# Optimization experiments

Measured on AMD Instinct MI355X. Metric: run time of the kernel, lower is better.

## Reference

```python
import jax, jax.numpy as jnp
import numpy as np

N_BLADES = 8  # Cl(3,0): 1, e1, e2, e3 and their products (bitmask blade indexing)


def _blade_sign(a: int, b: int) -> int:
    # Sign from reordering basis vectors when multiplying blades a*b (Euclidean metric).
    a >>= 1
    s = 0
    while a:
        s += bin(a & b).count('1')
        a >>= 1
    return -1 if (s & 1) else 1


def make_cayley() -> np.ndarray:
    C = np.zeros((N_BLADES, N_BLADES, N_BLADES), dtype=np.float32)
    for a in range(N_BLADES):
        for b in range(N_BLADES):
            C[a, b, a ^ b] = float(_blade_sign(a, b))
    return C


def setup_inputs() -> dict:
    key = jax.random.key(0)
    k1, k2 = jax.random.split(key)
    B, Cin, Cout = 8192, 256, 256
    scale = 1.0 / np.sqrt(Cin * N_BLADES)
    x = jax.random.normal(k1, (B, Cin, N_BLADES), dtype=jnp.float32)
    weight = jax.random.normal(k2, (Cout, Cin, N_BLADES), dtype=jnp.float32) * scale
    bias = jnp.zeros((Cout, N_BLADES), dtype=jnp.float32)
    cayley = jnp.asarray(make_cayley())
    return {"x": x, "weight": weight, "bias": bias, "cayley": cayley}


def reference(x, weight, bias, cayley):
    # A[b,o,j,k] = sum_i W[o,i,j] * X[b,i,k]  (weight blade j times input blade k)
    A = jnp.einsum('oij,bik->bojk', weight, x)
    # Contract blade pair (j,k) into output blade l via sparse Cayley table.
    out = jnp.einsum('jkl,bojk->bol', cayley, A)
    return out + bias[None, :, :]
```

## Files before the change

kernel.cpp:

```cpp
#include <hip/hip_runtime.h>
#include <stdint.h>
#include <stddef.h>


typedef __bf16 bf16x8  __attribute__((ext_vector_type(8)));
typedef float  f32x4   __attribute__((ext_vector_type(4)));

#define BM 256
#define BN 256
#define KSLICE 32
#define NSLICES 64
#define SLOT_ELEMS (256 * 32)

__device__ __forceinline__ void async_copy16(void* lds_dst, const void* g_src) {
    __builtin_amdgcn_global_load_lds(
        (__attribute__((address_space(1))) void*)g_src,
        (__attribute__((address_space(3))) void*)lds_dst,
        16, 0, 0);
}

__global__ __launch_bounds__(256) void prep_kernel(
    const float* __restrict__ x, __bf16* __restrict__ Xb, long nx,
    const float* __restrict__ W, const float* __restrict__ cayley,
    __bf16* __restrict__ Wt, int Cin, int Cout, int castBlocks)
{
    __shared__ float Cay[512];
    if ((int)blockIdx.x < castBlocks) {
        long i = ((long)blockIdx.x * 256 + threadIdx.x) * 8;
        if (i + 8 <= nx) {
            const f32x4* p = (const f32x4*)(x + i);
            f32x4 v0 = p[0];
            f32x4 v1 = p[1];
            bf16x8 o;
            o[0] = (__bf16)v0[0]; o[1] = (__bf16)v0[1];
            o[2] = (__bf16)v0[2]; o[3] = (__bf16)v0[3];
            o[4] = (__bf16)v1[0]; o[5] = (__bf16)v1[1];
            o[6] = (__bf16)v1[2]; o[7] = (__bf16)v1[3];
            *(bf16x8*)(Xb + i) = o;
        }
        return;
    }
    for (int t = threadIdx.x; t < 512; t += 256) Cay[t] = cayley[t];
    __syncthreads();

    int flat = (blockIdx.x - castBlocks) * 256 + threadIdx.x;
    int total = Cout * 8 * Cin;
    if (flat >= total) return;
    int i = flat % Cin;
    int n = flat / Cin;
    int o = n >> 3, l = n & 7;

    const float* wrow = W + ((size_t)o * Cin + i) * 8;
    float w8[8];
    #pragma unroll
    for (int j = 0; j < 8; ++j) w8[j] = wrow[j];

    bf16x8 outv;
    #pragma unroll
    for (int k = 0; k < 8; ++k) {
        float s = 0.f;
        #pragma unroll
        for (int j = 0; j < 8; ++j) s += Cay[j * 64 + k * 8 + l] * w8[j];
        outv[k] = (__bf16)s;
    }
    *(bf16x8*)(Wt + (size_t)n * (Cin * 8) + i * 8) = outv;
}

__global__ __launch_bounds__(512, 2) void gemm_bt_kernel(
    const __bf16* __restrict__ A,
    const __bf16* __restrict__ Bt,
    const float*  __restrict__ bias,
    float* __restrict__ C,
    int M, int N, int K)
{
    __shared__ __align__(16) __bf16 As[4][SLOT_ELEMS];
    __shared__ __align__(16) __bf16 Bs[4][SLOT_ELEMS];

    const int tid  = threadIdx.x;
    const int wave = tid >> 6;
    const int lane = tid & 63;
    const int quad = lane >> 4;
    const int l16  = lane & 15;

    const int bid = blockIdx.x;
    const int xcd = bid & 7;
    const int idx = bid >> 3;
    const int mBase = (xcd * 4 + (idx & 3)) * BM;
    const int nBase = (idx >> 2) * BN;

    const int srow = lane >> 2;
    const int sgrp = (lane & 3) ^ ((lane >> 3) & 3);
    const __bf16* gA0 = A  + (size_t)(mBase + wave * 32 +  0 + srow) * K + sgrp * 8;
    const __bf16* gA1 = A  + (size_t)(mBase + wave * 32 + 16 + srow) * K + sgrp * 8;
    const __bf16* gB0 = Bt + (size_t)(nBase + wave * 32 +  0 + srow) * K + sgrp * 8;
    const __bf16* gB1 = Bt + (size_t)(nBase + wave * 32 + 16 + srow) * K + sgrp * 8;
    const int stOff = wave * 1024;

#define STAGE_A(slot, q) do {                                             \
        async_copy16(&As[slot][stOff      ], gA0 + (size_t)(q) * KSLICE); \
        async_copy16(&As[slot][stOff + 512], gA1 + (size_t)(q) * KSLICE); \
    } while (0)
#define STAGE_B(slot, q) do {                                             \
        async_copy16(&Bs[slot][stOff      ], gB0 + (size_t)(q) * KSLICE); \
        async_copy16(&Bs[slot][stOff + 512], gB1 + (size_t)(q) * KSLICE); \
    } while (0)

    const int wm = wave >> 2;
    const int wn = wave & 3;
    const int offq = (quad ^ ((l16 >> 1) & 3)) * 8;
    const __bf16* paBase = &As[0][(wm * 128 + l16) * KSLICE + offq];
    const __bf16* pbBase = &Bs[0][(wn * 64  + l16) * KSLICE + offq];

    f32x4 acc[8][4] = {};
    bf16x8 af0A[4], bfA[4], af0B[4], bfB[4], af1[4];

    STAGE_A(0, 0); STAGE_B(0, 0);
    STAGE_A(1, 1); STAGE_B(1, 1);
    STAGE_A(2, 2); STAGE_B(2, 2);
    STAGE_B(3, 3);
    asm volatile("s_waitcnt vmcnt(10)" ::: "memory");
    __builtin_amdgcn_s_barrier();

    #pragma unroll
    for (int j = 0; j < 4; ++j)
        af0A[j] = *(const bf16x8*)(paBase + j * 512);
    #pragma unroll
    for (int j = 0; j < 4; ++j)
        bfA[j]  = *(const bf16x8*)(pbBase + j * 512);

#define SLICE_BODY(s_, c_, n_, AF0, BF, NAF0, NBF, DOA, DOB, DOPF)             \
    do {                                                                       \
        _Pragma("unroll")                                                      \
        for (int j = 0; j < 4; ++j)                                            \
            af1[j] = *(const bf16x8*)(paBase + (c_) * SLOT_ELEMS + (4 + j) * 512); \
        if (DOA) STAGE_A(((s_) + 3) & 3, (s_) + 3);                            \
        __builtin_amdgcn_s_setprio(1);                                         \
        _Pragma("unroll")                                                      \
        for (int j = 0; j < 4; ++j)                                            \
            _Pragma("unroll")                                                  \
            for (int n = 0; n < 4; ++n)                                        \
                acc[j][n] = __builtin_amdgcn_mfma_f32_16x16x32_bf16(           \
                    AF0[j], BF[n], acc[j][n], 0, 0, 0);                        \
        __builtin_amdgcn_s_setprio(0);                                         \
        asm volatile("s_waitcnt vmcnt(8)" ::: "memory");                       \
        __builtin_amdgcn_s_barrier();                                          \
        if (DOPF) {                                                            \
            _Pragma("unroll")                                                  \
            for (int j = 0; j < 4; ++j)                                        \
                NAF0[j] = *(const bf16x8*)(paBase + (n_) * SLOT_ELEMS + j * 512); \
            _Pragma("unroll")                                                  \
            for (int j = 0; j < 4; ++j)                                        \
                NBF[j] = *(const bf16x8*)(pbBase + (n_) * SLOT_ELEMS + j * 512); \
        }                                                                      \
        if (DOB) STAGE_B((s_) & 3, (s_) + 4);                                  \
        __builtin_amdgcn_s_setprio(1);                                         \
        _Pragma("unroll")                                                      \
        for (int j = 0; j < 4; ++j)                                            \
            _Pragma("unroll")                                                  \
            for (int n = 0; n < 4; ++n)                                        \
                acc[4 + j][n] = __builtin_amdgcn_mfma_f32_16x16x32_bf16(       \
                    af1[j], BF[n], acc[4 + j][n], 0, 0, 0);                    \
        __builtin_amdgcn_s_setprio(0);                                         \
        __builtin_amdgcn_s_barrier();                                          \
    } while (0)

    #pragma unroll 1
    for (int s4 = 0; s4 < 15; ++s4) {
        const int s = s4 * 4;
        SLICE_BODY(s + 0, 0, 1, af0A, bfA, af0B, bfB, true, true, true);
        SLICE_BODY(s + 1, 1, 2, af0B, bfB, af0A, bfA, true, true, true);
        SLICE_BODY(s + 2, 2, 3, af0A, bfA, af0B, bfB, true, true, true);
        SLICE_BODY(s + 3, 3, 0, af0B, bfB, af0A, bfA, true, true, true);
    }
    SLICE_BODY(60, 0, 1, af0A, bfA, af0B, bfB, true,  false, true);
    SLICE_BODY(61, 1, 2, af0B, bfB, af0A, bfA, false, false, true);
    SLICE_BODY(62, 2, 3, af0A, bfA, af0B, bfB, false, false, true);
    SLICE_BODY(63, 3, 0, af0B, bfB, af0A, bfA, false, false, false);
    asm volatile("s_waitcnt vmcnt(0)" ::: "memory");

#undef SLICE_BODY
#undef STAGE_A
#undef STAGE_B

    float bv[4];
    #pragma unroll
    for (int n = 0; n < 4; ++n)
        bv[n] = bias[nBase + wn * 64 + n * 16 + l16];

    #pragma unroll
    for (int m = 0; m < 8; ++m) {
        #pragma unroll
        for (int n = 0; n < 4; ++n) {
            const int col = nBase + wn * 64 + n * 16 + l16;
            #pragma unroll
            for (int r = 0; r < 4; ++r) {
                const int row = mBase + wm * 128 + m * 16 + quad * 4 + r;
                C[(size_t)row * N + col] = acc[m][n][r] + bv[n];
            }
        }
    }
}

extern "C" void kernel_launch(void* const* d_in, const int* in_sizes, int n_in,
                              void* d_out, int out_size, void* d_ws, size_t ws_size,
                              hipStream_t stream) {
    const float* x      = (const float*)d_in[0];
    const float* weight = (const float*)d_in[1];
    const float* bias   = (const float*)d_in[2];
    const float* cayley = (const float*)d_in[3];
    float* out = (float*)d_out;

    const int Cout = in_sizes[2] / 8;
    const int Cin  = in_sizes[1] / (Cout * 8);
    const int Bm   = in_sizes[0] / (Cin * 8);
    const int M = Bm;
    const int N = Cout * 8;
    const int K = Cin * 8;

    __bf16* Xb = (__bf16*)d_ws;
    __bf16* Wt = (__bf16*)((char*)d_ws + (size_t)M * K * 2);

    long nx = (long)M * K;
    int castBlocks = (int)(nx / 8 / 256);
    int foldBlocks = (N * Cin + 255) / 256;
    prep_kernel<<<castBlocks + foldBlocks, 256, 0, stream>>>(
        x, Xb, nx, weight, cayley, Wt, Cin, Cout, castBlocks);

    int grid = (M / BM) * (N / BN);
    gemm_bt_kernel<<<grid, 512, 0, stream>>>(Xb, Wt, bias, out, M, N, K);
}
```

Before: 176.4 us.

## Shrink GEMM tile to 256x128 with 256 threads and a 3-stage LDS pipeline

The block tile shrinks from 256x256 to 256x128 and the block from 512 to 256 threads, so each wave now stages four A row-groups. The LDS ring drops from four slots to three, with the prologue, prefetch distance, slot indexing and vmcnt waits rewritten to match. Total LDS per block falls enough that two blocks fit per CU and the grid doubles, aiming at better occupancy and load balance. The cost is lower data reuse per block, more global and L2 traffic for A, and a shallower prefetch pipeline.

```diff
diff --git a/kernel.cpp b/kernel.cpp
--- a/kernel.cpp
+++ b/kernel.cpp
@@ -7,10 +7,11 @@
 typedef float  f32x4   __attribute__((ext_vector_type(4)));
 
 #define BM 256
-#define BN 256
+#define BN 128
 #define KSLICE 32
 #define NSLICES 64
-#define SLOT_ELEMS (256 * 32)
+#define A_SLOT (256 * 32)
+#define B_SLOT (128 * 32)
 
 __device__ __forceinline__ void async_copy16(void* lds_dst, const void* g_src) {
     __builtin_amdgcn_global_load_lds(
@@ -66,15 +67,15 @@
     *(bf16x8*)(Wt + (size_t)n * (Cin * 8) + i * 8) = outv;
 }
 
-__global__ __launch_bounds__(512, 2) void gemm_bt_kernel(
+__global__ __launch_bounds__(256, 2) void gemm_bt_kernel(
     const __bf16* __restrict__ A,
     const __bf16* __restrict__ Bt,
     const float*  __restrict__ bias,
     float* __restrict__ C,
     int M, int N, int K)
 {
-    __shared__ __align__(16) __bf16 As[4][SLOT_ELEMS];
-    __shared__ __align__(16) __bf16 Bs[4][SLOT_ELEMS];
+    __shared__ __align__(16) __bf16 As[3][A_SLOT];
+    __shared__ __align__(16) __bf16 Bs[3][B_SLOT];
 
     const int tid  = threadIdx.x;
     const int wave = tid >> 6;
@@ -90,23 +91,28 @@
 
     const int srow = lane >> 2;
     const int sgrp = (lane & 3) ^ ((lane >> 3) & 3);
-    const __bf16* gA0 = A  + (size_t)(mBase + wave * 32 +  0 + srow) * K + sgrp * 8;
-    const __bf16* gA1 = A  + (size_t)(mBase + wave * 32 + 16 + srow) * K + sgrp * 8;
+    const __bf16* gA0 = A  + (size_t)(mBase + wave * 64 +  0 + srow) * K + sgrp * 8;
+    const __bf16* gA1 = A  + (size_t)(mBase + wave * 64 + 16 + srow) * K + sgrp * 8;
+    const __bf16* gA2 = A  + (size_t)(mBase + wave * 64 + 32 + srow) * K + sgrp * 8;
+    const __bf16* gA3 = A  + (size_t)(mBase + wave * 64 + 48 + srow) * K + sgrp * 8;
     const __bf16* gB0 = Bt + (size_t)(nBase + wave * 32 +  0 + srow) * K + sgrp * 8;
     const __bf16* gB1 = Bt + (size_t)(nBase + wave * 32 + 16 + srow) * K + sgrp * 8;
-    const int stOff = wave * 1024;
-
-#define STAGE_A(slot, q) do {                                             \
-        async_copy16(&As[slot][stOff      ], gA0 + (size_t)(q) * KSLICE); \
-        async_copy16(&As[slot][stOff + 512], gA1 + (size_t)(q) * KSLICE); \
+    const int stA = wave * 2048;
+    const int stB = wave * 1024;
+
+#define STAGE_A(slot, q) do {                                               \
+        async_copy16(&As[slot][stA       ], gA0 + (size_t)(q) * KSLICE);    \
+        async_copy16(&As[slot][stA +  512], gA1 + (size_t)(q) * KSLICE);    \
+        async_copy16(&As[slot][stA + 1024], gA2 + (size_t)(q) * KSLICE);    \
+        async_copy16(&As[slot][stA + 1536], gA3 + (size_t)(q) * KSLICE);    \
     } while (0)
-#define STAGE_B(slot, q) do {                                             \
-        async_copy16(&Bs[slot][stOff      ], gB0 + (size_t)(q) * KSLICE); \
-        async_copy16(&Bs[slot][stOff + 512], gB1 + (size_t)(q) * KSLICE); \
+#define STAGE_B(slot, q) do {                                               \
+        async_copy16(&Bs[slot][stB       ], gB0 + (size_t)(q) * KSLICE);    \
+        async_copy16(&Bs[slot][stB +  512], gB1 + (size_t)(q) * KSLICE);    \
     } while (0)
 
-    const int wm = wave >> 2;
-    const int wn = wave & 3;
+    const int wm = wave >> 1;
+    const int wn = wave & 1;
     const int offq = (quad ^ ((l16 >> 1) & 3)) * 8;
     const __bf16* paBase = &As[0][(wm * 128 + l16) * KSLICE + offq];
     const __bf16* pbBase = &Bs[0][(wn * 64  + l16) * KSLICE + offq];
@@ -116,9 +122,7 @@
 
     STAGE_A(0, 0); STAGE_B(0, 0);
     STAGE_A(1, 1); STAGE_B(1, 1);
-    STAGE_A(2, 2); STAGE_B(2, 2);
-    STAGE_B(3, 3);
-    asm volatile("s_waitcnt vmcnt(10)" ::: "memory");
+    asm volatile("s_waitcnt vmcnt(6)" ::: "memory");
     __builtin_amdgcn_s_barrier();
 
     #pragma unroll
@@ -128,12 +132,12 @@
     for (int j = 0; j < 4; ++j)
         bfA[j]  = *(const bf16x8*)(pbBase + j * 512);
 
-#define SLICE_BODY(s_, c_, n_, AF0, BF, NAF0, NBF, DOA, DOB, DOPF)             \
+#define SLICE_BODY(s_, c_, n_, AF0, BF, NAF0, NBF, DOA, DOB, DOPF, VM0)        \
     do {                                                                       \
         _Pragma("unroll")                                                      \
         for (int j = 0; j < 4; ++j)                                            \
-            af1[j] = *(const bf16x8*)(paBase + (c_) * SLOT_ELEMS + (4 + j) * 512); \
-        if (DOA) STAGE_A(((s_) + 3) & 3, (s_) + 3);                            \
+            af1[j] = *(const bf16x8*)(paBase + (c_) * A_SLOT + (4 + j) * 512); \
+        if (DOA) STAGE_A(((s_) + 2) % 3, (s_) + 2);                            \
         __builtin_amdgcn_s_setprio(1);                                         \
         _Pragma("unroll")                                                      \
         for (int j = 0; j < 4; ++j)                                            \
@@ -142,17 +146,18 @@
                 acc[j][n] = __builtin_amdgcn_mfma_f32_16x16x32_bf16(           \
                     AF0[j], BF[n], acc[j][n], 0, 0, 0);                        \
         __builtin_amdgcn_s_setprio(0);                                         \
-        asm volatile("s_waitcnt vmcnt(8)" ::: "memory");                       \
+        if (VM0) asm volatile("s_waitcnt vmcnt(0)" ::: "memory");              \
+        else     asm volatile("s_waitcnt vmcnt(4)" ::: "memory");              \
         __builtin_amdgcn_s_barrier();                                          \
         if (DOPF) {                                                            \
             _Pragma("unroll")                                                  \
             for (int j = 0; j < 4; ++j)                                        \
-                NAF0[j] = *(const bf16x8*)(paBase + (n_) * SLOT_ELEMS + j * 512); \
+                NAF0[j] = *(const bf16x8*)(paBase + (n_) * A_SLOT + j * 512);  \
             _Pragma("unroll")                                                  \
             for (int j = 0; j < 4; ++j)                                        \
-                NBF[j] = *(const bf16x8*)(pbBase + (n_) * SLOT_ELEMS + j * 512); \
+                NBF[j] = *(const bf16x8*)(pbBase + (n_) * B_SLOT + j * 512);   \
         }                                                                      \
-        if (DOB) STAGE_B((s_) & 3, (s_) + 4);                                  \
+        if (DOB) STAGE_B(((s_) + 2) % 3, (s_) + 2);                            \
         __builtin_amdgcn_s_setprio(1);                                         \
         _Pragma("unroll")                                                      \
         for (int j = 0; j < 4; ++j)                                            \
@@ -165,18 +170,18 @@
     } while (0)
 
     #pragma unroll 1
-    for (int s4 = 0; s4 < 15; ++s4) {
-        const int s = s4 * 4;
-        SLICE_BODY(s + 0, 0, 1, af0A, bfA, af0B, bfB, true, true, true);
-        SLICE_BODY(s + 1, 1, 2, af0B, bfB, af0A, bfA, true, true, true);
-        SLICE_BODY(s + 2, 2, 3, af0A, bfA, af0B, bfB, true, true, true);
-        SLICE_BODY(s + 3, 3, 0, af0B, bfB, af0A, bfA, true, true, true);
-    }
-    SLICE_BODY(60, 0, 1, af0A, bfA, af0B, bfB, true,  false, true);
-    SLICE_BODY(61, 1, 2, af0B, bfB, af0A, bfA, false, false, true);
-    SLICE_BODY(62, 2, 3, af0A, bfA, af0B, bfB, false, false, true);
-    SLICE_BODY(63, 3, 0, af0B, bfB, af0A, bfA, false, false, false);
-    asm volatile("s_waitcnt vmcnt(0)" ::: "memory");
+    for (int t = 0; t < 10; ++t) {
+        SLICE_BODY(6 * t + 0, 0, 1, af0A, bfA, af0B, bfB, true, true, true, false);
+        SLICE_BODY(6 * t + 1, 1, 2, af0B, bfB, af0A, bfA, true, true, true, false);
+        SLICE_BODY(6 * t + 2, 2, 0, af0A, bfA, af0B, bfB, true, true, true, false);
+        SLICE_BODY(6 * t + 3, 0, 1, af0B, bfB, af0A, bfA, true, true, true, false);
+        SLICE_BODY(6 * t + 4, 1, 2, af0A, bfA, af0B, bfB, true, true, true, false);
+        SLICE_BODY(6 * t + 5, 2, 0, af0B, bfB, af0A, bfA, true, true, true, false);
+    }
+    SLICE_BODY(60, 0, 1, af0A, bfA, af0B, bfB, true,  true,  true,  false);
+    SLICE_BODY(61, 1, 2, af0B, bfB, af0A, bfA, true,  true,  true,  false);
+    SLICE_BODY(62, 2, 0, af0A, bfA, af0B, bfB, false, false, true,  true);
+    SLICE_BODY(63, 0, 1, af0B, bfB, af0A, bfA, false, false, false, false);
 
 #undef SLICE_BODY
 #undef STAGE_A
@@ -227,5 +232,5 @@
         x, Xb, nx, weight, cayley, Wt, Cin, Cout, castBlocks);
 
     int grid = (M / BM) * (N / BN);
-    gemm_bt_kernel<<<grid, 512, 0, stream>>>(Xb, Wt, bias, out, M, N, K);
-}
+    gemm_bt_kernel<<<grid, 256, 0, stream>>>(Xb, Wt, bias, out, M, N, K);
+}
```

Result: slower. 180.6 us (+2.4%).

## Switch GEMM to 32x32x16 MFMA with pre-tiled k-major operand layout

Applied to the files above, without the earlier changes.

The prep kernel now writes both activations and folded weights in a blocked layout: each 256-row tile holds contiguous 8-element k-groups, so a whole k-slice is one contiguous 16 KB chunk. The GEMM stages each slice with fully coalesced linear async copies into LDS, which removes the swizzled addressing. The inner product moves from 16x16x32 to 32x32x16 MFMA with 16-wide accumulators, cutting the number of LDS fragment reads per FLOP. The pipeline depth changes from 4 B-slices ahead to 3 slices for both A and B, with adjusted waitcnt values. The cost is that the cast path now goes through an LDS transpose, and the B prefetch lead is shorter.

```diff
diff --git a/kernel.cpp b/kernel.cpp
--- a/kernel.cpp
+++ b/kernel.cpp
@@ -3,14 +3,15 @@
 #include <stddef.h>
 
 
-typedef __bf16 bf16x8  __attribute__((ext_vector_type(8)));
-typedef float  f32x4   __attribute__((ext_vector_type(4)));
+typedef __bf16 bf16x4 __attribute__((ext_vector_type(4)));
+typedef __bf16 bf16x8 __attribute__((ext_vector_type(8)));
+typedef float  f32x4  __attribute__((ext_vector_type(4)));
+typedef float  f32x16 __attribute__((ext_vector_type(16)));
 
 #define BM 256
 #define BN 256
-#define KSLICE 32
 #define NSLICES 64
-#define SLOT_ELEMS (256 * 32)
+#define SLOT 8192
 
 __device__ __forceinline__ void async_copy16(void* lds_dst, const void* g_src) {
     __builtin_amdgcn_global_load_lds(
@@ -20,34 +21,46 @@
 }
 
 __global__ __launch_bounds__(256) void prep_kernel(
-    const float* __restrict__ x, __bf16* __restrict__ Xb, long nx,
+    const float* __restrict__ x, __bf16* __restrict__ Xb2,
     const float* __restrict__ W, const float* __restrict__ cayley,
-    __bf16* __restrict__ Wt, int Cin, int Cout, int castBlocks)
+    __bf16* __restrict__ Wt2, int M, int N, int K, int Cin, int castBlocks)
 {
-    __shared__ float Cay[512];
     if ((int)blockIdx.x < castBlocks) {
-        long i = ((long)blockIdx.x * 256 + threadIdx.x) * 8;
-        if (i + 8 <= nx) {
-            const f32x4* p = (const f32x4*)(x + i);
-            f32x4 v0 = p[0];
-            f32x4 v1 = p[1];
-            bf16x8 o;
-            o[0] = (__bf16)v0[0]; o[1] = (__bf16)v0[1];
-            o[2] = (__bf16)v0[2]; o[3] = (__bf16)v0[3];
-            o[4] = (__bf16)v1[0]; o[5] = (__bf16)v1[1];
-            o[6] = (__bf16)v1[2]; o[7] = (__bf16)v1[3];
-            *(bf16x8*)(Xb + i) = o;
+        __shared__ __bf16 T[16 * 520];
+        const int tk = blockIdx.x & 15;
+        const int tm = blockIdx.x >> 4;
+        const int row0 = tm * 64, k0 = tk * 128;
+        #pragma unroll
+        for (int it = 0; it < 8; ++it) {
+            int idx = threadIdx.x + it * 256;
+            int r = idx >> 5, kq = idx & 31;
+            f32x4 v = *(const f32x4*)(x + (size_t)(row0 + r) * K + k0 + kq * 4);
+            bf16x4 b;
+            b[0] = (__bf16)v[0]; b[1] = (__bf16)v[1];
+            b[2] = (__bf16)v[2]; b[3] = (__bf16)v[3];
+            *(bf16x4*)&T[(kq >> 1) * 520 + r * 8 + (kq & 1) * 4] = b;
+        }
+        __syncthreads();
+        const size_t obase = (size_t)(row0 >> 8) * K * 256
+                           + (size_t)(k0 >> 3) * 2048
+                           + (size_t)(row0 & 255) * 8;
+        #pragma unroll
+        for (int it = 0; it < 4; ++it) {
+            int u = threadIdx.x + it * 256;
+            int koL = u >> 6, rowi = u & 63;
+            bf16x8 val = *(const bf16x8*)&T[koL * 520 + rowi * 8];
+            *(bf16x8*)(Xb2 + obase + (size_t)koL * 2048 + rowi * 8) = val;
         }
         return;
     }
+    __shared__ float Cay[512];
     for (int t = threadIdx.x; t < 512; t += 256) Cay[t] = cayley[t];
     __syncthreads();
 
-    int flat = (blockIdx.x - castBlocks) * 256 + threadIdx.x;
-    int total = Cout * 8 * Cin;
-    if (flat >= total) return;
-    int i = flat % Cin;
-    int n = flat / Cin;
+    int flat = ((int)blockIdx.x - castBlocks) * 256 + threadIdx.x;
+    if (flat >= Cin * N) return;
+    int n = flat % N;
+    int i = flat / N;
     int o = n >> 3, l = n & 7;
 
     const float* wrow = W + ((size_t)o * Cin + i) * 8;
@@ -63,24 +76,25 @@
         for (int j = 0; j < 8; ++j) s += Cay[j * 64 + k * 8 + l] * w8[j];
         outv[k] = (__bf16)s;
     }
-    *(bf16x8*)(Wt + (size_t)n * (Cin * 8) + i * 8) = outv;
+    *(bf16x8*)(Wt2 + (size_t)(n >> 8) * K * 256 + (size_t)i * 2048
+                   + (n & 255) * 8) = outv;
 }
 
 __global__ __launch_bounds__(512, 2) void gemm_bt_kernel(
-    const __bf16* __restrict__ A,
-    const __bf16* __restrict__ Bt,
+    const __bf16* __restrict__ A2,
+    const __bf16* __restrict__ B2,
     const float*  __restrict__ bias,
     float* __restrict__ C,
     int M, int N, int K)
 {
-    __shared__ __align__(16) __bf16 As[4][SLOT_ELEMS];
-    __shared__ __align__(16) __bf16 Bs[4][SLOT_ELEMS];
+    __shared__ __align__(16) __bf16 As[4][SLOT];
+    __shared__ __align__(16) __bf16 Bs[4][SLOT];
 
     const int tid  = threadIdx.x;
     const int wave = tid >> 6;
     const int lane = tid & 63;
-    const int quad = lane >> 4;
-    const int l16  = lane & 15;
+    const int l31  = lane & 31;
+    const int lhi  = lane >> 5;
 
     const int bid = blockIdx.x;
     const int xcd = bid & 7;
@@ -88,78 +102,79 @@
     const int mBase = (xcd * 4 + (idx & 3)) * BM;
     const int nBase = (idx >> 2) * BN;
 
-    const int srow = lane >> 2;
-    const int sgrp = (lane & 3) ^ ((lane >> 3) & 3);
-    const __bf16* gA0 = A  + (size_t)(mBase + wave * 32 +  0 + srow) * K + sgrp * 8;
-    const __bf16* gA1 = A  + (size_t)(mBase + wave * 32 + 16 + srow) * K + sgrp * 8;
-    const __bf16* gB0 = Bt + (size_t)(nBase + wave * 32 +  0 + srow) * K + sgrp * 8;
-    const __bf16* gB1 = Bt + (size_t)(nBase + wave * 32 + 16 + srow) * K + sgrp * 8;
-    const int stOff = wave * 1024;
-
-#define STAGE_A(slot, q) do {                                             \
-        async_copy16(&As[slot][stOff      ], gA0 + (size_t)(q) * KSLICE); \
-        async_copy16(&As[slot][stOff + 512], gA1 + (size_t)(q) * KSLICE); \
+    const int c0 = 2 * wave, c1 = 2 * wave + 1;
+    const __bf16* gA0 = A2 + (size_t)mBase * K + c0 * 512 + lane * 8;
+    const __bf16* gA1 = A2 + (size_t)mBase * K + c1 * 512 + lane * 8;
+    const __bf16* gB0 = B2 + (size_t)nBase * K + c0 * 512 + lane * 8;
+    const __bf16* gB1 = B2 + (size_t)nBase * K + c1 * 512 + lane * 8;
+    const int dstA0 = c0 * 512, dstA1 = c1 * 512;
+
+#define STAGE_A(slot, q) do {                                              \
+        async_copy16(&As[slot][dstA0], gA0 + (size_t)(q) * 8192);          \
+        async_copy16(&As[slot][dstA1], gA1 + (size_t)(q) * 8192);          \
     } while (0)
-#define STAGE_B(slot, q) do {                                             \
-        async_copy16(&Bs[slot][stOff      ], gB0 + (size_t)(q) * KSLICE); \
-        async_copy16(&Bs[slot][stOff + 512], gB1 + (size_t)(q) * KSLICE); \
+#define STAGE_B(slot, q) do {                                              \
+        async_copy16(&Bs[slot][dstA0], gB0 + (size_t)(q) * 8192);          \
+        async_copy16(&Bs[slot][dstA1], gB1 + (size_t)(q) * 8192);          \
     } while (0)
 
     const int wm = wave >> 2;
     const int wn = wave & 3;
-    const int offq = (quad ^ ((l16 >> 1) & 3)) * 8;
-    const __bf16* paBase = &As[0][(wm * 128 + l16) * KSLICE + offq];
-    const __bf16* pbBase = &Bs[0][(wn * 64  + l16) * KSLICE + offq];
-
-    f32x4 acc[8][4] = {};
-    bf16x8 af0A[4], bfA[4], af0B[4], bfB[4], af1[4];
+    const __bf16* paBase = &As[0][lhi * 2048 + (wm * 128 + l31) * 8];
+    const __bf16* pbBase = &Bs[0][lhi * 2048 + (wn * 64  + l31) * 8];
+
+    f32x16 acc[4][2] = {};
+    bf16x8 a0A[4], b0A[2], a0B[4], b0B[2], af1[4], bf1[2];
 
     STAGE_A(0, 0); STAGE_B(0, 0);
     STAGE_A(1, 1); STAGE_B(1, 1);
     STAGE_A(2, 2); STAGE_B(2, 2);
-    STAGE_B(3, 3);
-    asm volatile("s_waitcnt vmcnt(10)" ::: "memory");
+    asm volatile("s_waitcnt vmcnt(8)" ::: "memory");
     __builtin_amdgcn_s_barrier();
 
     #pragma unroll
     for (int j = 0; j < 4; ++j)
-        af0A[j] = *(const bf16x8*)(paBase + j * 512);
-    #pragma unroll
-    for (int j = 0; j < 4; ++j)
-        bfA[j]  = *(const bf16x8*)(pbBase + j * 512);
-
-#define SLICE_BODY(s_, c_, n_, AF0, BF, NAF0, NBF, DOA, DOB, DOPF)             \
+        a0A[j] = *(const bf16x8*)(paBase + j * 256);
+    #pragma unroll
+    for (int q = 0; q < 2; ++q)
+        b0A[q] = *(const bf16x8*)(pbBase + q * 256);
+
+#define SLICE_BODY(s_, c_, n_, A0F, B0F, A0N, B0N, DOA, DOB, DOPF, VM0)        \
     do {                                                                       \
         _Pragma("unroll")                                                      \
         for (int j = 0; j < 4; ++j)                                            \
-            af1[j] = *(const bf16x8*)(paBase + (c_) * SLOT_ELEMS + (4 + j) * 512); \
+            af1[j] = *(const bf16x8*)(paBase + (c_) * SLOT + 4096 + j * 256);  \
+        _Pragma("unroll")                                                      \
+        for (int q = 0; q < 2; ++q)                                            \
+            bf1[q] = *(const bf16x8*)(pbBase + (c_) * SLOT + 4096 + q * 256);  \
         if (DOA) STAGE_A(((s_) + 3) & 3, (s_) + 3);                            \
         __builtin_amdgcn_s_setprio(1);                                         \
         _Pragma("unroll")                                                      \
         for (int j = 0; j < 4; ++j)                                            \
             _Pragma("unroll")                                                  \
-            for (int n = 0; n < 4; ++n)                                        \
-                acc[j][n] = __builtin_amdgcn_mfma_f32_16x16x32_bf16(           \
-                    AF0[j], BF[n], acc[j][n], 0, 0, 0);                        \
+            for (int q = 0; q < 2; ++q)                                        \
+                acc[j][q] = __builtin_amdgcn_mfma_f32_32x32x16_bf16(           \
+                    A0F[j], B0F[q], acc[j][q], 0, 0, 0);                       \
         __builtin_amdgcn_s_setprio(0);                                         \
-        asm volatile("s_waitcnt vmcnt(8)" ::: "memory");                       \
+        if (VM0) asm volatile("s_waitcnt vmcnt(0)" ::: "memory");              \
+        else     asm volatile("s_waitcnt vmcnt(6)" ::: "memory");              \
         __builtin_amdgcn_s_barrier();                                          \
         if (DOPF) {                                                            \
             _Pragma("unroll")                                                  \
             for (int j = 0; j < 4; ++j)                                        \
-                NAF0[j] = *(const bf16x8*)(paBase + (n_) * SLOT_ELEMS + j * 512); \
-            _Pragma("unroll")                                                  \
-            for (int j = 0; j < 4; ++j)                                        \
-                NBF[j] = *(const bf16x8*)(pbBase + (n_) * SLOT_ELEMS + j * 512); \
+                A0N[j] = *(const bf16x8*)(paBase + (n_) * SLOT + j * 256);     \
+            _Pragma("unroll")                                                  \
+            for (int q = 0; q < 2; ++q)                                        \
+                B0N[q] = *(const bf16x8*)(pbBase + (n_) * SLOT + q * 256);     \
         }                                                                      \
-        if (DOB) STAGE_B((s_) & 3, (s_) + 4);                                  \
+        if (DOB) STAGE_B(((s_) + 3) & 3, (s_) + 3);                            \
         __builtin_amdgcn_s_setprio(1);                                         \
         _Pragma("unroll")                                                      \
         for (int j = 0; j < 4; ++j)                                            \
             _Pragma("unroll")                                                  \
-            for (int n = 0; n < 4; ++n)                                        \
-                acc[4 + j][n] = __builtin_amdgcn_mfma_f32_16x16x32_bf16(       \
-                    af1[j], BF[n], acc[4 + j][n], 0, 0, 0);                    \
+            for (int q = 0; q < 2; ++q)                                        \
+                acc[j][q] = __builtin_amdgcn_mfma_f32_32x32x16_bf16(           \
+                    af1[j], bf1[q], acc[j][q], 0, 0, 0);                       \
         __builtin_amdgcn_s_setprio(0);                                         \
         __builtin_amdgcn_s_barrier();                                          \
     } while (0)
@@ -167,35 +182,36 @@
     #pragma unroll 1
     for (int s4 = 0; s4 < 15; ++s4) {
         const int s = s4 * 4;
-        SLICE_BODY(s + 0, 0, 1, af0A, bfA, af0B, bfB, true, true, true);
-        SLICE_BODY(s + 1, 1, 2, af0B, bfB, af0A, bfA, true, true, true);
-        SLICE_BODY(s + 2, 2, 3, af0A, bfA, af0B, bfB, true, true, true);
-        SLICE_BODY(s + 3, 3, 0, af0B, bfB, af0A, bfA, true, true, true);
-    }
-    SLICE_BODY(60, 0, 1, af0A, bfA, af0B, bfB, true,  false, true);
-    SLICE_BODY(61, 1, 2, af0B, bfB, af0A, bfA, false, false, true);
-    SLICE_BODY(62, 2, 3, af0A, bfA, af0B, bfB, false, false, true);
-    SLICE_BODY(63, 3, 0, af0B, bfB, af0A, bfA, false, false, false);
+        SLICE_BODY(s + 0, 0, 1, a0A, b0A, a0B, b0B, true, true, true, false);
+        SLICE_BODY(s + 1, 1, 2, a0B, b0B, a0A, b0A, true, true, true, false);
+        SLICE_BODY(s + 2, 2, 3, a0A, b0A, a0B, b0B, true, true, true, false);
+        SLICE_BODY(s + 3, 3, 0, a0B, b0B, a0A, b0A, true, true, true, false);
+    }
+    SLICE_BODY(60, 0, 1, a0A, b0A, a0B, b0B, true,  true,  true,  false);
+    SLICE_BODY(61, 1, 2, a0B, b0B, a0A, b0A, false, false, true,  true);
+    SLICE_BODY(62, 2, 3, a0A, b0A, a0B, b0B, false, false, true,  true);
+    SLICE_BODY(63, 3, 0, a0B, b0B, a0A, b0A, false, false, false, true);
     asm volatile("s_waitcnt vmcnt(0)" ::: "memory");
 
 #undef SLICE_BODY
 #undef STAGE_A
 #undef STAGE_B
 
-    float bv[4];
-    #pragma unroll
-    for (int n = 0; n < 4; ++n)
-        bv[n] = bias[nBase + wn * 64 + n * 16 + l16];
-
-    #pragma unroll
-    for (int m = 0; m < 8; ++m) {
-        #pragma unroll
-        for (int n = 0; n < 4; ++n) {
-            const int col = nBase + wn * 64 + n * 16 + l16;
+    float bv[2];
+    #pragma unroll
+    for (int q = 0; q < 2; ++q)
+        bv[q] = bias[nBase + wn * 64 + q * 32 + l31];
+
+    #pragma unroll
+    for (int mt = 0; mt < 4; ++mt) {
+        #pragma unroll
+        for (int q = 0; q < 2; ++q) {
+            const int col = nBase + wn * 64 + q * 32 + l31;
             #pragma unroll
-            for (int r = 0; r < 4; ++r) {
-                const int row = mBase + wm * 128 + m * 16 + quad * 4 + r;
-                C[(size_t)row * N + col] = acc[m][n][r] + bv[n];
+            for (int r = 0; r < 16; ++r) {
+                const int row = mBase + wm * 128 + mt * 32
+                              + (r & 3) + 8 * (r >> 2) + 4 * lhi;
+                C[(size_t)row * N + col] = acc[mt][q][r] + bv[q];
             }
         }
     }
@@ -217,15 +233,14 @@
     const int N = Cout * 8;
     const int K = Cin * 8;
 
-    __bf16* Xb = (__bf16*)d_ws;
-    __bf16* Wt = (__bf16*)((char*)d_ws + (size_t)M * K * 2);
-
-    long nx = (long)M * K;
-    int castBlocks = (int)(nx / 8 / 256);
-    int foldBlocks = (N * Cin + 255) / 256;
+    __bf16* Xb2 = (__bf16*)d_ws;
+    __bf16* Wt2 = (__bf16*)((char*)d_ws + (size_t)M * K * 2);
+
+    int castBlocks = (M / 64) * (K / 128);
+    int foldBlocks = (Cin * N + 255) / 256;
     prep_kernel<<<castBlocks + foldBlocks, 256, 0, stream>>>(
-        x, Xb, nx, weight, cayley, Wt, Cin, Cout, castBlocks);
+        x, Xb2, weight, cayley, Wt2, M, N, K, Cin, castBlocks);
 
     int grid = (M / BM) * (N / BN);
-    gemm_bt_kernel<<<grid, 512, 0, stream>>>(Xb, Wt, bias, out, M, N, K);
-}
+    gemm_bt_kernel<<<grid, 512, 0, stream>>>(Xb2, Wt2, bias, out, M, N, K);
+}
```

After: 181.7 us. 1.03x slower.

## Restructure GEMM mainloop into 8-phase quadrant schedule with 64-wide K tiles

Applied to the files above, without the earlier changes.

Replaces the 4-slot, 32-wide K-slice pipeline with a double-buffered scheme using 64-wide K tiles split into M and N halves. Each K tile is processed in four phases over output quadrants, and half-tile loads for the next stage are interleaved into every phase. The wave-to-output mapping changes to interleaved 64x32 sub-blocks per half, and the LDS swizzle is updated to match. This aims to spread global-to-LDS traffic evenly and to cut LDS fragment reloads per MFMA, at the cost of more barriers and a more intricate vmcnt accounting that could stall if it is wrong.

```diff
diff --git a/kernel.cpp b/kernel.cpp
--- a/kernel.cpp
+++ b/kernel.cpp
@@ -3,14 +3,11 @@
 #include <stddef.h>
 
 
-typedef __bf16 bf16x8  __attribute__((ext_vector_type(8)));
-typedef float  f32x4   __attribute__((ext_vector_type(4)));
+typedef __bf16 bf16x8 __attribute__((ext_vector_type(8)));
+typedef float  f32x4  __attribute__((ext_vector_type(4)));
 
 #define BM 256
 #define BN 256
-#define KSLICE 32
-#define NSLICES 64
-#define SLOT_ELEMS (256 * 32)
 
 __device__ __forceinline__ void async_copy16(void* lds_dst, const void* g_src) {
     __builtin_amdgcn_global_load_lds(
@@ -73,8 +70,8 @@
     float* __restrict__ C,
     int M, int N, int K)
 {
-    __shared__ __align__(16) __bf16 As[4][SLOT_ELEMS];
-    __shared__ __align__(16) __bf16 Bs[4][SLOT_ELEMS];
+    __shared__ __align__(16) __bf16 AS[2 * 2 * 8192];
+    __shared__ __align__(16) __bf16 BS[2 * 2 * 8192];
 
     const int tid  = threadIdx.x;
     const int wave = tid >> 6;
@@ -88,115 +85,121 @@
     const int mBase = (xcd * 4 + (idx & 3)) * BM;
     const int nBase = (idx >> 2) * BN;
 
-    const int srow = lane >> 2;
-    const int sgrp = (lane & 3) ^ ((lane >> 3) & 3);
-    const __bf16* gA0 = A  + (size_t)(mBase + wave * 32 +  0 + srow) * K + sgrp * 8;
-    const __bf16* gA1 = A  + (size_t)(mBase + wave * 32 + 16 + srow) * K + sgrp * 8;
-    const __bf16* gB0 = Bt + (size_t)(nBase + wave * 32 +  0 + srow) * K + sgrp * 8;
-    const __bf16* gB1 = Bt + (size_t)(nBase + wave * 32 + 16 + srow) * K + sgrp * 8;
-    const int stOff = wave * 1024;
-
-#define STAGE_A(slot, q) do {                                             \
-        async_copy16(&As[slot][stOff      ], gA0 + (size_t)(q) * KSLICE); \
-        async_copy16(&As[slot][stOff + 512], gA1 + (size_t)(q) * KSLICE); \
+    const int rsub = lane >> 3;
+    const int colE = ((lane & 7) ^ rsub) * 8;
+    const int c0 = 2 * wave, c1 = 2 * wave + 1;
+    const __bf16* pA0 = A  + (size_t)(mBase + c0 * 8 + rsub) * K + colE;
+    const __bf16* pA1 = A  + (size_t)(mBase + c1 * 8 + rsub) * K + colE;
+    const __bf16* pB0 = Bt + (size_t)(nBase + c0 * 8 + rsub) * K + colE;
+    const __bf16* pB1 = Bt + (size_t)(nBase + c1 * 8 + rsub) * K + colE;
+
+#define STAGE_A(SB, SH, SKT) do {                                              \
+        async_copy16(&AS[((SB) * 2 + (SH)) * 8192 + c0 * 512],                 \
+                     pA0 + (size_t)(SH) * 128 * K + (size_t)(SKT) * 64);       \
+        async_copy16(&AS[((SB) * 2 + (SH)) * 8192 + c1 * 512],                 \
+                     pA1 + (size_t)(SH) * 128 * K + (size_t)(SKT) * 64);       \
     } while (0)
-#define STAGE_B(slot, q) do {                                             \
-        async_copy16(&Bs[slot][stOff      ], gB0 + (size_t)(q) * KSLICE); \
-        async_copy16(&Bs[slot][stOff + 512], gB1 + (size_t)(q) * KSLICE); \
+#define STAGE_B(SB, SH, SKT) do {                                              \
+        async_copy16(&BS[((SB) * 2 + (SH)) * 8192 + c0 * 512],                 \
+                     pB0 + (size_t)(SH) * 128 * K + (size_t)(SKT) * 64);       \
+        async_copy16(&BS[((SB) * 2 + (SH)) * 8192 + c1 * 512],                 \
+                     pB1 + (size_t)(SH) * 128 * K + (size_t)(SKT) * 64);       \
     } while (0)
 
     const int wm = wave >> 2;
     const int wn = wave & 3;
-    const int offq = (quad ^ ((l16 >> 1) & 3)) * 8;
-    const __bf16* paBase = &As[0][(wm * 128 + l16) * KSLICE + offq];
-    const __bf16* pbBase = &Bs[0][(wn * 64  + l16) * KSLICE + offq];
+    const int aRd = wm * 4096 + l16 * 64 + ((quad ^ (l16 & 7)) * 8);
+    const int bRd = wn * 2048 + l16 * 64 + ((quad ^ (l16 & 7)) * 8);
 
     f32x4 acc[8][4] = {};
-    bf16x8 af0A[4], bfA[4], af0B[4], bfB[4], af1[4];
-
-    STAGE_A(0, 0); STAGE_B(0, 0);
-    STAGE_A(1, 1); STAGE_B(1, 1);
-    STAGE_A(2, 2); STAGE_B(2, 2);
-    STAGE_B(3, 3);
-    asm volatile("s_waitcnt vmcnt(10)" ::: "memory");
-    __builtin_amdgcn_s_barrier();
-
-    #pragma unroll
-    for (int j = 0; j < 4; ++j)
-        af0A[j] = *(const bf16x8*)(paBase + j * 512);
-    #pragma unroll
-    for (int j = 0; j < 4; ++j)
-        bfA[j]  = *(const bf16x8*)(pbBase + j * 512);
-
-#define SLICE_BODY(s_, c_, n_, AF0, BF, NAF0, NBF, DOA, DOB, DOPF)             \
+    bf16x8 af[4][2], bfr[2][2];
+
+#define PHASE(BUF, MH, NH, RDA, RDB, ST, SB, SH, SKT, VM)                      \
     do {                                                                       \
-        _Pragma("unroll")                                                      \
-        for (int j = 0; j < 4; ++j)                                            \
-            af1[j] = *(const bf16x8*)(paBase + (c_) * SLOT_ELEMS + (4 + j) * 512); \
-        if (DOA) STAGE_A(((s_) + 3) & 3, (s_) + 3);                            \
+        if (RDA) {                                                             \
+            _Pragma("unroll")                                                  \
+            for (int mf = 0; mf < 4; ++mf)                                     \
+                _Pragma("unroll")                                              \
+                for (int kk = 0; kk < 2; ++kk)                                 \
+                    af[mf][kk] = *(const bf16x8*)(AS + ((BUF)*2+(MH))*8192     \
+                                    + ((aRd ^ (kk*32)) + mf*1024));            \
+        }                                                                      \
+        if (RDB) {                                                             \
+            _Pragma("unroll")                                                  \
+            for (int nf = 0; nf < 2; ++nf)                                     \
+                _Pragma("unroll")                                              \
+                for (int kk = 0; kk < 2; ++kk)                                 \
+                    bfr[nf][kk] = *(const bf16x8*)(BS + ((BUF)*2+(NH))*8192    \
+                                    + ((bRd ^ (kk*32)) + nf*1024));            \
+        }                                                                      \
+        if ((ST) == 1) STAGE_A(SB, SH, SKT);                                   \
+        else if ((ST) == 2) STAGE_B(SB, SH, SKT);                              \
+        __builtin_amdgcn_s_barrier();                                          \
+        asm volatile("s_waitcnt lgkmcnt(0)" ::: "memory");                     \
         __builtin_amdgcn_s_setprio(1);                                         \
         _Pragma("unroll")                                                      \
-        for (int j = 0; j < 4; ++j)                                            \
+        for (int mf = 0; mf < 4; ++mf)                                         \
             _Pragma("unroll")                                                  \
-            for (int n = 0; n < 4; ++n)                                        \
-                acc[j][n] = __builtin_amdgcn_mfma_f32_16x16x32_bf16(           \
-                    AF0[j], BF[n], acc[j][n], 0, 0, 0);                        \
+            for (int nf = 0; nf < 2; ++nf)                                     \
+                _Pragma("unroll")                                              \
+                for (int kk = 0; kk < 2; ++kk)                                 \
+                    acc[(MH)*4+mf][(NH)*2+nf] =                                \
+                        __builtin_amdgcn_mfma_f32_16x16x32_bf16(               \
+                            af[mf][kk], bfr[nf][kk],                           \
+                            acc[(MH)*4+mf][(NH)*2+nf], 0, 0, 0);               \
         __builtin_amdgcn_s_setprio(0);                                         \
-        asm volatile("s_waitcnt vmcnt(8)" ::: "memory");                       \
-        __builtin_amdgcn_s_barrier();                                          \
-        if (DOPF) {                                                            \
-            _Pragma("unroll")                                                  \
-            for (int j = 0; j < 4; ++j)                                        \
-                NAF0[j] = *(const bf16x8*)(paBase + (n_) * SLOT_ELEMS + j * 512); \
-            _Pragma("unroll")                                                  \
-            for (int j = 0; j < 4; ++j)                                        \
-                NBF[j] = *(const bf16x8*)(pbBase + (n_) * SLOT_ELEMS + j * 512); \
-        }                                                                      \
-        if (DOB) STAGE_B((s_) & 3, (s_) + 4);                                  \
-        __builtin_amdgcn_s_setprio(1);                                         \
-        _Pragma("unroll")                                                      \
-        for (int j = 0; j < 4; ++j)                                            \
-            _Pragma("unroll")                                                  \
-            for (int n = 0; n < 4; ++n)                                        \
-                acc[4 + j][n] = __builtin_amdgcn_mfma_f32_16x16x32_bf16(       \
-                    af1[j], BF[n], acc[4 + j][n], 0, 0, 0);                    \
-        __builtin_amdgcn_s_setprio(0);                                         \
+        if ((VM) == 6)      asm volatile("s_waitcnt vmcnt(6)" ::: "memory");   \
+        else if ((VM) == 0) asm volatile("s_waitcnt vmcnt(0)" ::: "memory");   \
         __builtin_amdgcn_s_barrier();                                          \
     } while (0)
 
+    STAGE_A(0, 0, 0); STAGE_B(0, 0, 0); STAGE_B(0, 1, 0); STAGE_A(0, 1, 0);
+    STAGE_A(1, 0, 1); STAGE_B(1, 1, 1); STAGE_A(1, 1, 1);
+    asm volatile("s_waitcnt vmcnt(6)" ::: "memory");
+    __builtin_amdgcn_s_barrier();
+
     #pragma unroll 1
-    for (int s4 = 0; s4 < 15; ++s4) {
-        const int s = s4 * 4;
-        SLICE_BODY(s + 0, 0, 1, af0A, bfA, af0B, bfB, true, true, true);
-        SLICE_BODY(s + 1, 1, 2, af0B, bfB, af0A, bfA, true, true, true);
-        SLICE_BODY(s + 2, 2, 3, af0A, bfA, af0B, bfB, true, true, true);
-        SLICE_BODY(s + 3, 3, 0, af0B, bfB, af0A, bfA, true, true, true);
-    }
-    SLICE_BODY(60, 0, 1, af0A, bfA, af0B, bfB, true,  false, true);
-    SLICE_BODY(61, 1, 2, af0B, bfB, af0A, bfA, false, false, true);
-    SLICE_BODY(62, 2, 3, af0A, bfA, af0B, bfB, false, false, true);
-    SLICE_BODY(63, 3, 0, af0B, bfB, af0A, bfA, false, false, false);
+    for (int t = 0; t < 15; ++t) {
+        const int kt = 2 * t;
+        PHASE(0, 0, 0, 1, 1, 2, 1, 0, kt + 1, -1);
+        PHASE(0, 0, 1, 0, 1, 1, 0, 0, kt + 2, -1);
+        PHASE(0, 1, 1, 1, 0, 2, 0, 1, kt + 2, -1);
+        PHASE(0, 1, 0, 0, 1, 1, 0, 1, kt + 2,  6);
+        PHASE(1, 0, 0, 1, 1, 2, 0, 0, kt + 2, -1);
+        PHASE(1, 0, 1, 0, 1, 1, 1, 0, kt + 3, -1);
+        PHASE(1, 1, 1, 1, 0, 2, 1, 1, kt + 3, -1);
+        PHASE(1, 1, 0, 0, 1, 1, 1, 1, kt + 3,  6);
+    }
+    PHASE(0, 0, 0, 1, 1, 2, 1, 0, 31, -1);
+    PHASE(0, 0, 1, 0, 1, 0, 0, 0, 0, -1);
+    PHASE(0, 1, 1, 1, 0, 0, 0, 0, 0, -1);
+    PHASE(0, 1, 0, 0, 1, 0, 0, 0, 0,  0);
+    PHASE(1, 0, 0, 1, 1, 0, 0, 0, 0, -1);
+    PHASE(1, 0, 1, 0, 1, 0, 0, 0, 0, -1);
+    PHASE(1, 1, 1, 1, 0, 0, 0, 0, 0, -1);
+    PHASE(1, 1, 0, 0, 1, 0, 0, 0, 0, -1);
     asm volatile("s_waitcnt vmcnt(0)" ::: "memory");
 
-#undef SLICE_BODY
+#undef PHASE
 #undef STAGE_A
 #undef STAGE_B
 
     float bv[4];
     #pragma unroll
-    for (int n = 0; n < 4; ++n)
-        bv[n] = bias[nBase + wn * 64 + n * 16 + l16];
-
-    #pragma unroll
-    for (int m = 0; m < 8; ++m) {
+    for (int bj = 0; bj < 4; ++bj)
+        bv[bj] = bias[nBase + (bj >> 1) * 128 + wn * 32 + (bj & 1) * 16 + l16];
+
+    #pragma unroll
+    for (int ai = 0; ai < 8; ++ai) {
+        const int row0 = mBase + (ai >> 2) * 128 + wm * 64 + (ai & 3) * 16
+                       + quad * 4;
         #pragma unroll
-        for (int n = 0; n < 4; ++n) {
-            const int col = nBase + wn * 64 + n * 16 + l16;
+        for (int bj = 0; bj < 4; ++bj) {
+            const int col = nBase + (bj >> 1) * 128 + wn * 32 + (bj & 1) * 16
+                          + l16;
             #pragma unroll
-            for (int r = 0; r < 4; ++r) {
-                const int row = mBase + wm * 128 + m * 16 + quad * 4 + r;
-                C[(size_t)row * N + col] = acc[m][n][r] + bv[n];
-            }
+            for (int r = 0; r < 4; ++r)
+                C[(size_t)(row0 + r) * N + col] = acc[ai][bj][r] + bv[bj];
         }
     }
 }
```

Measured after the change: 181.4 us. 1.03x slower.
